# Optimization experiments

Measured on AMD Instinct MI355X. Metric: run time of the kernel, lower is better.

The kernel has to match this reference:

```python
import jax, jax.numpy as jnp
import numpy as np

EPS = 1e-5  # torch LayerNorm default eps
B, N, D_IN, E, H, V = 4096, 32, 256, 128, 512, 32

def _ln(x):
    # LayerNorm without affine (elementwise_affine=False), biased variance
    m = jnp.mean(x, axis=-1, keepdims=True)
    v = jnp.mean(jnp.square(x - m), axis=-1, keepdims=True)
    return (x - m) * jax.lax.rsqrt(v + EPS)

def _ln_gru_cell(x, h, i2h_W, i2h_b, h2h_W, h2h_b, hW_W, hW_b, hU_W, hU_b):
    gates = jax.nn.sigmoid(_ln(x @ i2h_W + i2h_b) + _ln(h @ h2h_W + h2h_b))  # [B,2H]
    hs = h.shape[-1]
    z_t = gates[:, :hs]
    r_t = gates[:, hs:]
    h_hat = jnp.tanh(_ln(x @ hW_W + hW_b) + r_t * _ln(h @ hU_W + hU_b))
    return (1.0 - z_t) * h + z_t * h_hat

def setup_inputs() -> dict:
    key = jax.random.key(0)
    ks = jax.random.split(key, 32)
    std0 = 1.0 / np.sqrt(H)
    u = lambda k, shp: jax.random.uniform(k, shp, jnp.float32, -std0, std0)
    in0 = 3 * E  # attn context + msg embedding + feedback embedding
    inp = {
        'sender_messages_embedded': jax.random.normal(ks[0], (B, E), jnp.float32),
        'prev_hidden': jax.random.normal(ks[1], (2, B, H), jnp.float32),
        'candidate_objects': jax.random.normal(ks[2], (B, N, D_IN), jnp.float32),
        'prev_msg_embedding': jax.random.normal(ks[3], (B, E), jnp.float32),
        # linear_objects_in_keys
        'Wk': jax.random.normal(ks[4], (D_IN, E), jnp.float32) * 0.05,
        'bk': jnp.zeros((E,), jnp.float32),
        # LayerNormGRUCell layer 0 (input 3E)
        'i2h_W0': u(ks[5], (in0, 2 * H)), 'i2h_b0': u(ks[6], (2 * H,)),
        'h2h_W0': u(ks[7], (H, 2 * H)), 'h2h_b0': u(ks[8], (2 * H,)),
        'hW_W0': u(ks[9], (in0, H)), 'hW_b0': u(ks[10], (H,)),
        'hU_W0': u(ks[11], (H, H)), 'hU_b0': u(ks[12], (H,)),
        # LayerNormGRUCell layer 1 (input H)
        'i2h_W1': u(ks[13], (H, 2 * H)), 'i2h_b1': u(ks[14], (2 * H,)),
        'h2h_W1': u(ks[15], (H, 2 * H)), 'h2h_b1': u(ks[16], (2 * H,)),
        'hW_W1': u(ks[17], (H, H)), 'hW_b1': u(ks[18], (H,)),
        'hU_W1': u(ks[19], (H, H)), 'hU_b1': u(ks[20], (H,)),
        # hidden_to_feedback_output
        'out_W': jax.random.normal(ks[21], (H, V), jnp.float32) * 0.05,
        'out_b': jnp.zeros((V,), jnp.float32),
    }
    return inp

def reference(sender_messages_embedded, prev_hidden, candidate_objects, prev_msg_embedding,
              Wk, bk,
              i2h_W0, i2h_b0, h2h_W0, h2h_b0, hW_W0, hW_b0, hU_W0, hU_b0,
              i2h_W1, i2h_b1, h2h_W1, h2h_b1, hW_W1, hW_b1, hU_W1, hU_b1,
              out_W, out_b):
    # object attention (dot): query = msg embedding, keys = projected candidates
    keys = candidate_objects @ Wk + bk                              # [B,N,E]
    scores = jnp.einsum('be,bne->bn', sender_messages_embedded, keys)
    weights = jax.nn.softmax(scores, axis=1)                        # [B,N]
    context = jnp.einsum('bn,bne->be', weights, keys)               # [B,E]
    rnn_input = jnp.concatenate([context, sender_messages_embedded, prev_msg_embedding], axis=-1)  # [B,3E]
    h0 = _ln_gru_cell(rnn_input, prev_hidden[0], i2h_W0, i2h_b0, h2h_W0, h2h_b0, hW_W0, hW_b0, hU_W0, hU_b0)
    h1 = _ln_gru_cell(h0, prev_hidden[1], i2h_W1, i2h_b1, h2h_W1, h2h_b1, hW_W1, hW_b1, hU_W1, hU_b1)
    logits = h1 @ out_W + out_b                                     # [B,V]
    logp = jax.nn.log_softmax(logits, axis=-1)
    probs = jnp.exp(logp)
    entropy = -jnp.sum(probs * logp, axis=-1)                       # [B]
    output_token = jnp.argmax(probs, axis=-1)                       # eval-mode argmax
    output_token_logits = jnp.take_along_axis(logp, output_token[:, None], axis=1)[:, 0]
    new_hidden = jnp.stack([h0, h1])                                # [2,B,H]
    return (output_token, entropy, output_token_logits, logits, new_hidden)
```

## Files before the change

kernel.cpp:

```cpp
#include <hip/hip_runtime.h>
#include <hip/hip_bf16.h>
#include <math.h>

#define B_SZ   4096
#define NCAND  32
#define DIN    256
#define E_SZ   128
#define H_SZ   512
#define VOCAB  32
#define LN_EPS 1e-5f

typedef unsigned short u16;
typedef unsigned int   u32;
typedef __attribute__((ext_vector_type(8))) short  short8;
typedef __attribute__((ext_vector_type(4))) float  floatx4;

static __device__ __forceinline__ float sigmoidf_(float x) {
    return 1.0f / (1.0f + expf(-x));
}
static __device__ __forceinline__ u16 f2bf(float x) {
    u32 u = __float_as_uint(x);
    return (u16)((u + 0x7FFFu + ((u >> 16) & 1u)) >> 16);
}
static __device__ __forceinline__ float bfbits2f(u16 h) {
    return __uint_as_float(((u32)h) << 16);
}

static __device__ __forceinline__ void split_store8(const float* __restrict__ g,
                                                    u16* __restrict__ sh,
                                                    u16* __restrict__ sl)
{
    float4 a = *(const float4*)g;
    float4 b = *(const float4*)(g + 4);
    float v[8] = {a.x, a.y, a.z, a.w, b.x, b.y, b.z, b.w};
    union { u16 us[8]; uint4 q; } hb, lb;
    #pragma unroll
    for (int j = 0; j < 8; ++j) {
        u16 h = f2bf(v[j]);
        hb.us[j] = h;
        lb.us[j] = f2bf(v[j] - bfbits2f(h));
    }
    *(uint4*)sh = hb.q;
    *(uint4*)sl = lb.q;
}

__global__ __launch_bounds__(256)
void transpose_split_w(const float* __restrict__ W1, const float* __restrict__ W2,
                       int N1, int N2, int K,
                       u16* __restrict__ Wt_hi, u16* __restrict__ Wt_lo)
{
    __shared__ float t[64][68];
    const int n0 = blockIdx.x * 64, k0 = blockIdx.y * 64;
    const int tid = threadIdx.x;

    {
        const int kl = tid >> 4, nl4 = (tid & 15) * 4;
        const int ng = n0 + nl4;
        const float* src; int col, ld;
        if (ng < N1) { src = W1; col = ng;      ld = N1; }
        else         { src = W2; col = ng - N1; ld = N2; }
        #pragma unroll
        for (int p = 0; p < 4; ++p) {
            float4 v = *(const float4*)(src + (size_t)(k0 + kl + p * 16) * ld + col);
            *(float4*)&t[kl + p * 16][nl4] = v;
        }
    }
    __syncthreads();

    const int nl = tid >> 2, kc = tid & 3;
    union { u16 us[16]; uint4 v[2]; } hb, lb;
    #pragma unroll
    for (int j = 0; j < 16; ++j) {
        float x = t[kc * 16 + j][nl];
        u16 h = f2bf(x);
        float r = x - bfbits2f(h);
        hb.us[j] = h;
        lb.us[j] = f2bf(r);
    }
    const size_t off = (size_t)(n0 + nl) * K + k0 + kc * 16;
    *(uint4*)(Wt_hi + off)     = hb.v[0];
    *(uint4*)(Wt_hi + off + 8) = hb.v[1];
    *(uint4*)(Wt_lo + off)     = lb.v[0];
    *(uint4*)(Wt_lo + off + 8) = lb.v[1];
}

__global__ __launch_bounds__(256)
void bias_cat_kernel(const float* __restrict__ b1, const float* __restrict__ b2,
                     int N1, int Ntot, float* __restrict__ out)
{
    int i = blockIdx.x * 256 + threadIdx.x;
    if (i < Ntot) out[i] = (i < N1) ? b1[i] : b2[i - N1];
}

__global__ __launch_bounds__(256)
void mfma_gemm_dual_kernel(const float* __restrict__ Ax, const u16* __restrict__ Wxh,
                           const u16* __restrict__ Wxl, const float* __restrict__ bx,
                           float* __restrict__ Cx, int Kx,
                           const float* __restrict__ Ahp, const u16* __restrict__ Whh,
                           const u16* __restrict__ Whl, const float* __restrict__ bh,
                           float* __restrict__ Ch, int Kh)
{
    __shared__ u16 sAh[128 * 40];
    __shared__ u16 sAl[128 * 40];
    __shared__ u16 sWh[128 * 40];
    __shared__ u16 sWl[128 * 40];

    const int tid  = threadIdx.x;
    const int lane = tid & 63;
    const int wave = tid >> 6;
    const int wm = (wave >> 1) * 64;
    const int wn = (wave & 1) * 64;
    const int r16 = lane & 15;
    const int q8  = (lane >> 4) * 8;

    const int sel    = blockIdx.y >> 5;
    const int m_base = (blockIdx.y & 31) * 128;
    const int n_base = blockIdx.x * 128;

    const float* A    = sel ? Ahp : Ax;
    const u16*   Wth  = sel ? Whh : Wxh;
    const u16*   Wtl  = sel ? Whl : Wxl;
    const float* bias = sel ? bh  : bx;
    float*       C    = sel ? Ch  : Cx;
    const int    K    = sel ? Kh  : Kx;

    const int row0 = tid >> 2,         col0 = (tid & 3) * 8;
    const int row1 = (tid + 256) >> 2, col1 = ((tid + 256) & 3) * 8;

    floatx4 acc[4][4] = {};

    for (int k0 = 0; k0 < K; k0 += 32) {
        {
            split_store8(A + (size_t)(m_base + row0) * K + k0 + col0,
                         &sAh[row0 * 40 + col0], &sAl[row0 * 40 + col0]);
            split_store8(A + (size_t)(m_base + row1) * K + k0 + col1,
                         &sAh[row1 * 40 + col1], &sAl[row1 * 40 + col1]);
            const size_t gW0 = (size_t)(n_base + row0) * K + k0 + col0;
            const size_t gW1 = (size_t)(n_base + row1) * K + k0 + col1;
            *(uint4*)&sWh[row0 * 40 + col0] = *(const uint4*)(Wth + gW0);
            *(uint4*)&sWh[row1 * 40 + col1] = *(const uint4*)(Wth + gW1);
            *(uint4*)&sWl[row0 * 40 + col0] = *(const uint4*)(Wtl + gW0);
            *(uint4*)&sWl[row1 * 40 + col1] = *(const uint4*)(Wtl + gW1);
        }
        __syncthreads();

        short8 ah[4], al[4], bhf[4], blf[4];
        #pragma unroll
        for (int i = 0; i < 4; ++i) {
            const int ar = (wm + i * 16 + r16) * 40 + q8;
            ah[i] = *(const short8*)&sAh[ar];
            al[i] = *(const short8*)&sAl[ar];
            const int br = (wn + i * 16 + r16) * 40 + q8;
            bhf[i] = *(const short8*)&sWh[br];
            blf[i] = *(const short8*)&sWl[br];
        }
        #pragma unroll
        for (int i = 0; i < 4; ++i)
            #pragma unroll
            for (int j = 0; j < 4; ++j) {
                acc[i][j] = __builtin_amdgcn_mfma_f32_16x16x32_bf16(ah[i], bhf[j], acc[i][j], 0, 0, 0);
                acc[i][j] = __builtin_amdgcn_mfma_f32_16x16x32_bf16(ah[i], blf[j], acc[i][j], 0, 0, 0);
                acc[i][j] = __builtin_amdgcn_mfma_f32_16x16x32_bf16(al[i], bhf[j], acc[i][j], 0, 0, 0);
            }
        __syncthreads();
    }

    const int quad = lane >> 4;
    #pragma unroll
    for (int j = 0; j < 4; ++j) {
        const int n = n_base + wn + j * 16 + r16;
        const float bv = bias[n];
        #pragma unroll
        for (int i = 0; i < 4; ++i) {
            #pragma unroll
            for (int r = 0; r < 4; ++r) {
                const int m = m_base + wm + i * 16 + quad * 4 + r;
                C[(size_t)m * 1536 + n] = acc[i][j][r] + bv;
            }
        }
    }
}

__global__ __launch_bounds__(256)
void gemm_bt64_kernel(const float* __restrict__ A, const float* __restrict__ Bt,
                      float* __restrict__ C, int M, int N, int K, int ldc)
{
    __shared__ float As[16][68];
    __shared__ float Bs[16][68];

    const int tid = threadIdx.x;
    const int bm = blockIdx.y * 64;
    const int bn = blockIdx.x * 64;
    const int tx = tid & 15, ty = tid >> 4;
    const int m0 = ty * 4, n0 = tx * 4;
    const int arow = tid >> 2, acol = (tid & 3) * 4;

    float acc[4][4] = {};

    for (int k0 = 0; k0 < K; k0 += 16) {
        float4 a4 = *(const float4*)(A  + (size_t)(bm + arow) * K + (k0 + acol));
        float4 b4 = *(const float4*)(Bt + (size_t)(bn + arow) * K + (k0 + acol));
        As[acol + 0][arow] = a4.x; As[acol + 1][arow] = a4.y;
        As[acol + 2][arow] = a4.z; As[acol + 3][arow] = a4.w;
        Bs[acol + 0][arow] = b4.x; Bs[acol + 1][arow] = b4.y;
        Bs[acol + 2][arow] = b4.z; Bs[acol + 3][arow] = b4.w;
        __syncthreads();
        #pragma unroll
        for (int k = 0; k < 16; ++k) {
            float4 av = *(const float4*)&As[k][m0];
            float4 bv = *(const float4*)&Bs[k][n0];
            float aa[4] = {av.x, av.y, av.z, av.w};
            float bb[4] = {bv.x, bv.y, bv.z, bv.w};
            #pragma unroll
            for (int i = 0; i < 4; ++i)
                #pragma unroll
                for (int j = 0; j < 4; ++j)
                    acc[i][j] = fmaf(aa[i], bb[j], acc[i][j]);
        }
        __syncthreads();
    }

    #pragma unroll
    for (int i = 0; i < 4; ++i)
        *(float4*)(C + (size_t)(bm + m0 + i) * ldc + bn + n0) =
            make_float4(acc[i][0], acc[i][1], acc[i][2], acc[i][3]);
}

__global__ __launch_bounds__(256)
void attn_ctx_kernel(const float* __restrict__ co, const float* __restrict__ q,
                     const float* __restrict__ snd, const float* __restrict__ pmsg,
                     float* __restrict__ cbar, float* __restrict__ rnn_in)
{
    __shared__ float s_co[NCAND][264];
    __shared__ float s_q[DIN];
    __shared__ float s_scores[NCAND];
    __shared__ float s_w[NCAND];

    const int b   = blockIdx.x;
    const int tid = threadIdx.x;

    {
        const float4* cop = (const float4*)(co + (size_t)b * NCAND * DIN);
        #pragma unroll
        for (int i = 0; i < 8; ++i) {
            int idx = tid + i * 256;
            float4 v = cop[idx];
            *(float4*)&s_co[idx >> 6][(idx & 63) * 4] = v;
        }
        if (tid < DIN) s_q[tid] = q[(size_t)b * DIN + tid];
    }
    __syncthreads();

    {
        const int n = tid >> 3, part = tid & 7;
        float sc = 0.f;
        #pragma unroll
        for (int qq = 0; qq < 8; ++qq) {
            const int d = part * 4 + qq * 32;
            float4 cv = *(const float4*)&s_co[n][d];
            float4 qv = *(const float4*)&s_q[d];
            sc += cv.x * qv.x + cv.y * qv.y + cv.z * qv.z + cv.w * qv.w;
        }
        #pragma unroll
        for (int m = 4; m; m >>= 1) sc += __shfl_xor(sc, m);
        if (part == 0) s_scores[n] = sc;
    }
    __syncthreads();

    if (tid < NCAND) {
        float s  = s_scores[tid];
        float mx = s;
        #pragma unroll
        for (int m = 16; m; m >>= 1) mx = fmaxf(mx, __shfl_xor(mx, m));
        float e = expf(s - mx);
        float sum = e;
        #pragma unroll
        for (int m = 16; m; m >>= 1) sum += __shfl_xor(sum, m);
        s_w[tid] = e / sum;
    }
    __syncthreads();

    {
        float cb = 0.f;
        #pragma unroll
        for (int n = 0; n < NCAND; ++n) cb = fmaf(s_w[n], s_co[n][tid], cb);
        cbar[(size_t)b * DIN + tid] = cb;
    }
    if (tid < 128)
        rnn_in[(size_t)b * 384 + 128 + tid] = snd[(size_t)b * E_SZ + tid];
    else
        rnn_in[(size_t)b * 384 + 128 + tid] = pmsg[(size_t)b * E_SZ + (tid - 128)];
}

__global__ __launch_bounds__(256)
void gemm_ctx_kernel(const float* __restrict__ A, const float* __restrict__ Bm,
                     const float* __restrict__ bias, float* __restrict__ C,
                     int M, int N, int K, int ldc)
{
    __shared__ float As[16][132];
    __shared__ float Bs[16][68];

    const int tid = threadIdx.x;
    const int bm = blockIdx.y * 128;
    const int bn = blockIdx.x * 64;
    const int tx = tid & 15, ty = tid >> 4;
    const int m0 = ty * 8, n0 = tx * 4;
    const int arow = tid >> 1, acol = (tid & 1) * 8;
    const int brow = tid >> 4, bcol = (tid & 15) * 4;

    float acc[8][4] = {};

    for (int k0 = 0; k0 < K; k0 += 16) {
        float4 a0 = *(const float4*)(A + (size_t)(bm + arow) * K + (k0 + acol));
        float4 a1 = *(const float4*)(A + (size_t)(bm + arow) * K + (k0 + acol + 4));
        float4 b4 = *(const float4*)(Bm + (size_t)(k0 + brow) * N + (bn + bcol));
        As[acol + 0][arow] = a0.x; As[acol + 1][arow] = a0.y;
        As[acol + 2][arow] = a0.z; As[acol + 3][arow] = a0.w;
        As[acol + 4][arow] = a1.x; As[acol + 5][arow] = a1.y;
        As[acol + 6][arow] = a1.z; As[acol + 7][arow] = a1.w;
        *(float4*)&Bs[brow][bcol] = b4;
        __syncthreads();
        #pragma unroll
        for (int k = 0; k < 16; ++k) {
            float4 av0 = *(const float4*)&As[k][m0];
            float4 av1 = *(const float4*)&As[k][m0 + 4];
            float4 bv  = *(const float4*)&Bs[k][n0];
            float aa[8] = {av0.x, av0.y, av0.z, av0.w, av1.x, av1.y, av1.z, av1.w};
            float bb[4] = {bv.x, bv.y, bv.z, bv.w};
            #pragma unroll
            for (int i = 0; i < 8; ++i)
                #pragma unroll
                for (int j = 0; j < 4; ++j)
                    acc[i][j] = fmaf(aa[i], bb[j], acc[i][j]);
        }
        __syncthreads();
    }

    const float4 bv = *(const float4*)(bias + bn + n0);
    #pragma unroll
    for (int i = 0; i < 8; ++i) {
        float4 o;
        o.x = acc[i][0] + bv.x; o.y = acc[i][1] + bv.y;
        o.z = acc[i][2] + bv.z; o.w = acc[i][3] + bv.w;
        *(float4*)(C + (size_t)(bm + m0 + i) * ldc + bn + n0) = o;
    }
}

__global__ __launch_bounds__(256)
void gru_combine_kernel(const float* __restrict__ gxc, const float* __restrict__ ghc,
                        const float* __restrict__ hprev, float* __restrict__ hout)
{
    const int b    = blockIdx.x;
    const int tid  = threadIdx.x;
    const int lane = tid & 63, wv = tid >> 6;

    __shared__ float s_part[4][8];
    __shared__ float s_gates[1024];

    const float* gxb = gxc + (size_t)b * 1536;
    const float* ghb = ghc + (size_t)b * 1536;

    const float4 gx4 = *(const float4*)(gxb + tid * 4);
    const float4 gh4 = *(const float4*)(ghb + tid * 4);
    const float2 cx2 = *(const float2*)(gxb + 1024 + tid * 2);
    const float2 ch2 = *(const float2*)(ghb + 1024 + tid * 2);

    float v[8];
    v[0] = gx4.x + gx4.y + gx4.z + gx4.w;
    v[1] = gx4.x*gx4.x + gx4.y*gx4.y + gx4.z*gx4.z + gx4.w*gx4.w;
    v[2] = gh4.x + gh4.y + gh4.z + gh4.w;
    v[3] = gh4.x*gh4.x + gh4.y*gh4.y + gh4.z*gh4.z + gh4.w*gh4.w;
    v[4] = cx2.x + cx2.y;
    v[5] = cx2.x*cx2.x + cx2.y*cx2.y;
    v[6] = ch2.x + ch2.y;
    v[7] = ch2.x*ch2.x + ch2.y*ch2.y;

    #pragma unroll
    for (int i = 0; i < 8; ++i)
        #pragma unroll
        for (int m = 32; m; m >>= 1) v[i] += __shfl_xor(v[i], m);

    if (lane == 0) {
        #pragma unroll
        for (int i = 0; i < 8; ++i) s_part[wv][i] = v[i];
    }
    __syncthreads();

    float t[8];
    #pragma unroll
    for (int i = 0; i < 8; ++i)
        t[i] = s_part[0][i] + s_part[1][i] + s_part[2][i] + s_part[3][i];

    const float mgx = t[0] / 1024.f;
    const float rgx = 1.f / sqrtf(t[1] / 1024.f - mgx * mgx + LN_EPS);
    const float mgh = t[2] / 1024.f;
    const float rgh = 1.f / sqrtf(t[3] / 1024.f - mgh * mgh + LN_EPS);
    const float mcx = t[4] / 512.f;
    const float rcx = 1.f / sqrtf(t[5] / 512.f - mcx * mcx + LN_EPS);
    const float mch = t[6] / 512.f;
    const float rch = 1.f / sqrtf(t[7] / 512.f - mch * mch + LN_EPS);

    float4 g;
    g.x = sigmoidf_((gx4.x - mgx) * rgx + (gh4.x - mgh) * rgh);
    g.y = sigmoidf_((gx4.y - mgx) * rgx + (gh4.y - mgh) * rgh);
    g.z = sigmoidf_((gx4.z - mgx) * rgx + (gh4.z - mgh) * rgh);
    g.w = sigmoidf_((gx4.w - mgx) * rgx + (gh4.w - mgh) * rgh);
    *(float4*)&s_gates[tid * 4] = g;
    __syncthreads();

    const float2 hp2 = *(const float2*)(hprev + (size_t)b * 512 + tid * 2);
    const float z0 = s_gates[tid * 2 + 0];
    const float z1 = s_gates[tid * 2 + 1];
    const float r0 = s_gates[512 + tid * 2 + 0];
    const float r1 = s_gates[512 + tid * 2 + 1];

    const float hh0 = tanhf((cx2.x - mcx) * rcx + r0 * ((ch2.x - mch) * rch));
    const float hh1 = tanhf((cx2.y - mcx) * rcx + r1 * ((ch2.y - mch) * rch));
    const float hn0 = (1.f - z0) * hp2.x + z0 * hh0;
    const float hn1 = (1.f - z1) * hp2.y + z1 * hh1;

    *(float2*)(hout + (size_t)b * 512 + tid * 2) = make_float2(hn0, hn1);
}

__global__ __launch_bounds__(256)
void out_kernel(const float* __restrict__ h1, const float* __restrict__ W,
                const float* __restrict__ bias, float* __restrict__ out)
{
    __shared__ float s_h[4][512];
    const int wave = threadIdx.x >> 6, lane = threadIdx.x & 63;
    const int b = blockIdx.x * 4 + wave;

    {
        const float4* hp = (const float4*)(h1 + (size_t)b * 512);
        float4* sp = (float4*)&s_h[wave][0];
        sp[lane]      = hp[lane];
        sp[lane + 64] = hp[lane + 64];
    }
    __syncthreads();

    const int v = lane & 31, half = lane >> 5;
    float acc = 0.f;
    {
        const float* wp = W + (size_t)half * 256 * 32 + v;
        const float* hh = &s_h[wave][half * 256];
        for (int k = 0; k < 256; ++k) acc = fmaf(hh[k], wp[(size_t)k * 32], acc);
    }
    acc += __shfl_xor(acc, 32);
    const float logit = acc + bias[v];

    if (half == 0)
        out[(size_t)3 * B_SZ + (size_t)b * VOCAB + v] = logit;

    float mval = logit; int midx = v;
    #pragma unroll
    for (int m = 16; m; m >>= 1) {
        float ov = __shfl_xor(mval, m);
        int   oi = __shfl_xor(midx, m);
        if (ov > mval || (ov == mval && oi < midx)) { mval = ov; midx = oi; }
    }
    float ex = expf(logit - mval);
    float sum = ex;
    #pragma unroll
    for (int m = 16; m; m >>= 1) sum += __shfl_xor(sum, m);
    const float lse  = mval + logf(sum);
    const float logp = logit - lse;
    const float p    = expf(logp);
    float epl = p * logp;
    #pragma unroll
    for (int m = 16; m; m >>= 1) epl += __shfl_xor(epl, m);
    const float entropy = -epl;
    const float tok_logp = __shfl(logp, midx, 32);

    if (lane == 0) {
        out[b]             = (float)midx;
        out[B_SZ + b]      = entropy;
        out[2 * B_SZ + b]  = tok_logp;
    }
}

extern "C" void kernel_launch(void* const* d_in, const int* in_sizes, int n_in,
                              void* d_out, int out_size, void* d_ws, size_t ws_size,
                              hipStream_t stream)
{
    const float* snd    = (const float*)d_in[0];
    const float* ph     = (const float*)d_in[1];
    const float* co     = (const float*)d_in[2];
    const float* pmsg   = (const float*)d_in[3];
    const float* Wk     = (const float*)d_in[4];
    const float* bk     = (const float*)d_in[5];
    const float* i2hW0  = (const float*)d_in[6];
    const float* i2hb0  = (const float*)d_in[7];
    const float* h2hW0  = (const float*)d_in[8];
    const float* h2hb0  = (const float*)d_in[9];
    const float* hWW0   = (const float*)d_in[10];
    const float* hWb0   = (const float*)d_in[11];
    const float* hUW0   = (const float*)d_in[12];
    const float* hUb0   = (const float*)d_in[13];
    const float* i2hW1  = (const float*)d_in[14];
    const float* i2hb1  = (const float*)d_in[15];
    const float* h2hW1  = (const float*)d_in[16];
    const float* h2hb1  = (const float*)d_in[17];
    const float* hWW1   = (const float*)d_in[18];
    const float* hWb1   = (const float*)d_in[19];
    const float* hUW1   = (const float*)d_in[20];
    const float* hUb1   = (const float*)d_in[21];
    const float* outW   = (const float*)d_in[22];
    const float* outb   = (const float*)d_in[23];

    float* out = (float*)d_out;
    float* h0out = out + (size_t)3 * B_SZ + (size_t)B_SZ * VOCAB;
    float* h1out = h0out + (size_t)B_SZ * H_SZ;

    const float* h0prev = ph;
    const float* h1prev = ph + (size_t)B_SZ * H_SZ;

    char* p = (char*)d_ws;
    auto alloc_f = [&](size_t n) { float* r = (float*)p; p += n * 4; return r; };
    auto alloc_h = [&](size_t n) { u16* r = (u16*)p; p += ((n * 2 + 15) & ~15ull); return r; };

    float* qbuf   = alloc_f((size_t)B_SZ * 256);
    float* cbar   = alloc_f((size_t)B_SZ * 256);
    float* rnn_in = alloc_f((size_t)B_SZ * 384);
    float* gxc    = alloc_f((size_t)B_SZ * 1536);
    float* ghc    = alloc_f((size_t)B_SZ * 1536);
    u16* W0x_hi = alloc_h((size_t)1536 * 384);
    u16* W0x_lo = alloc_h((size_t)1536 * 384);
    u16* W0h_hi = alloc_h((size_t)1536 * 512);
    u16* W0h_lo = alloc_h((size_t)1536 * 512);
    u16* W1x_hi = alloc_h((size_t)1536 * 512);
    u16* W1x_lo = alloc_h((size_t)1536 * 512);
    u16* W1h_hi = alloc_h((size_t)1536 * 512);
    u16* W1h_lo = alloc_h((size_t)1536 * 512);
    float* b0x = alloc_f(1536);
    float* b0h = alloc_f(1536);
    float* b1x = alloc_f(1536);
    float* b1h = alloc_f(1536);

    transpose_split_w<<<dim3(24, 6), 256, 0, stream>>>(i2hW0, hWW0, 1024, 512, 384, W0x_hi, W0x_lo);
    transpose_split_w<<<dim3(24, 8), 256, 0, stream>>>(h2hW0, hUW0, 1024, 512, 512, W0h_hi, W0h_lo);
    transpose_split_w<<<dim3(24, 8), 256, 0, stream>>>(i2hW1, hWW1, 1024, 512, 512, W1x_hi, W1x_lo);
    transpose_split_w<<<dim3(24, 8), 256, 0, stream>>>(h2hW1, hUW1, 1024, 512, 512, W1h_hi, W1h_lo);
    bias_cat_kernel<<<6, 256, 0, stream>>>(i2hb0, hWb0, 1024, 1536, b0x);
    bias_cat_kernel<<<6, 256, 0, stream>>>(h2hb0, hUb0, 1024, 1536, b0h);
    bias_cat_kernel<<<6, 256, 0, stream>>>(i2hb1, hWb1, 1024, 1536, b1x);
    bias_cat_kernel<<<6, 256, 0, stream>>>(h2hb1, hUb1, 1024, 1536, b1h);

    gemm_bt64_kernel<<<dim3(4, 64), 256, 0, stream>>>(snd, Wk, qbuf, B_SZ, 256, 128, 256);
    attn_ctx_kernel<<<B_SZ, 256, 0, stream>>>(co, qbuf, snd, pmsg, cbar, rnn_in);
    gemm_ctx_kernel<<<dim3(2, 32), 256, 0, stream>>>(cbar, Wk, bk, rnn_in, B_SZ, 128, 256, 384);

    mfma_gemm_dual_kernel<<<dim3(12, 64), 256, 0, stream>>>(
        rnn_in, W0x_hi, W0x_lo, b0x, gxc, 384,
        ph,     W0h_hi, W0h_lo, b0h, ghc, 512);
    gru_combine_kernel<<<B_SZ, 256, 0, stream>>>(gxc, ghc, h0prev, h0out);

    mfma_gemm_dual_kernel<<<dim3(12, 64), 256, 0, stream>>>(
        h0out,                    W1x_hi, W1x_lo, b1x, gxc, 512,
        ph + (size_t)B_SZ * 512,  W1h_hi, W1h_lo, b1h, ghc, 512);
    gru_combine_kernel<<<B_SZ, 256, 0, stream>>>(gxc, ghc, h1prev, h1out);

    out_kernel<<<B_SZ / 4, 256, 0, stream>>>(h1out, outW, outb, out);
}
```

Before: 468.8 us.

## Pre-split GEMM operands into tile-blocked bf16 images loaded via global_load_lds

Activations (rnn input, previous hidden states, h0) are now split into bf16 hi/lo pairs by their producing kernels and stored in a 128x32 tile-blocked layout, so the dual MFMA GEMM no longer converts fp32 to bf16 in its main loop. The GEMM stages tiles with direct global-to-LDS loads and drops the padded LDS stride. The four bias concatenations are also merged into one launch. In exchange the producers do extra writes, an extra split kernel runs over prev_hidden, and the unpadded LDS rows may cause bank conflicts when fragments are read.

After: 452.3 us. 3.5% less time.

```diff
diff --git a/kernel.cpp b/kernel.cpp
--- a/kernel.cpp
+++ b/kernel.cpp
@@ -26,6 +26,12 @@
     return __uint_as_float(((u32)h) << 16);
 }
 
+typedef const __attribute__((address_space(1))) unsigned int* gas_ptr;
+typedef __attribute__((address_space(3)))       unsigned int* las_ptr;
+static __device__ __forceinline__ void gload_lds16(const u16* g, u16* l) {
+    __builtin_amdgcn_global_load_lds((gas_ptr)(const void*)g, (las_ptr)(void*)l, 16, 0, 0);
+}
+
 static __device__ __forceinline__ void split_store8(const float* __restrict__ g,
                                                     u16* __restrict__ sh,
                                                     u16* __restrict__ sl)
@@ -44,6 +50,7 @@
     *(uint4*)sl = lb.q;
 }
 
+
 __global__ __launch_bounds__(256)
 void transpose_split_w(const float* __restrict__ W1, const float* __restrict__ W2,
                        int N1, int N2, int K,
@@ -52,6 +59,7 @@
     __shared__ float t[64][68];
     const int n0 = blockIdx.x * 64, k0 = blockIdx.y * 64;
     const int tid = threadIdx.x;
+    const int KT = K >> 5;
 
     {
         const int kl = tid >> 4, nl4 = (tid & 15) * 4;
@@ -77,7 +85,10 @@
         hb.us[j] = h;
         lb.us[j] = f2bf(r);
     }
-    const size_t off = (size_t)(n0 + nl) * K + k0 + kc * 16;
+    const int n  = n0 + nl;
+    const int kb = k0 + kc * 16;
+    const size_t off = ((size_t)(n >> 7) * KT + (kb >> 5)) * 4096
+                     + (size_t)(n & 127) * 32 + (kb & 31);
     *(uint4*)(Wt_hi + off)     = hb.v[0];
     *(uint4*)(Wt_hi + off + 8) = hb.v[1];
     *(uint4*)(Wt_lo + off)     = lb.v[0];
@@ -85,25 +96,45 @@
 }
 
 __global__ __launch_bounds__(256)
-void bias_cat_kernel(const float* __restrict__ b1, const float* __restrict__ b2,
-                     int N1, int Ntot, float* __restrict__ out)
-{
-    int i = blockIdx.x * 256 + threadIdx.x;
-    if (i < Ntot) out[i] = (i < N1) ? b1[i] : b2[i - N1];
-}
-
-__global__ __launch_bounds__(256)
-void mfma_gemm_dual_kernel(const float* __restrict__ Ax, const u16* __restrict__ Wxh,
-                           const u16* __restrict__ Wxl, const float* __restrict__ bx,
-                           float* __restrict__ Cx, int Kx,
-                           const float* __restrict__ Ahp, const u16* __restrict__ Whh,
-                           const u16* __restrict__ Whl, const float* __restrict__ bh,
-                           float* __restrict__ Ch, int Kh)
-{
-    __shared__ u16 sAh[128 * 40];
-    __shared__ u16 sAl[128 * 40];
-    __shared__ u16 sWh[128 * 40];
-    __shared__ u16 sWl[128 * 40];
+void bias_cat4_kernel(const float* __restrict__ a0, const float* __restrict__ c0, float* __restrict__ o0,
+                      const float* __restrict__ a1, const float* __restrict__ c1, float* __restrict__ o1,
+                      const float* __restrict__ a2, const float* __restrict__ c2, float* __restrict__ o2,
+                      const float* __restrict__ a3, const float* __restrict__ c3, float* __restrict__ o3)
+{
+    const int t = blockIdx.x * 256 + threadIdx.x;
+    const int w = t / 1536;
+    const int i = t - w * 1536;
+    const float* a; const float* c; float* o;
+    if      (w == 0) { a = a0; c = c0; o = o0; }
+    else if (w == 1) { a = a1; c = c1; o = o1; }
+    else if (w == 2) { a = a2; c = c2; o = o2; }
+    else             { a = a3; c = c3; o = o3; }
+    o[i] = (i < 1024) ? a[i] : c[i - 1024];
+}
+
+__global__ __launch_bounds__(256)
+void split_blocked_kernel(const float* __restrict__ src,
+                          u16* __restrict__ hi, u16* __restrict__ lo)
+{
+    const int i = blockIdx.x * 256 + threadIdx.x;
+    const int m = i >> 6, kq = (i & 63) << 3;
+    const size_t idx = ((size_t)(m >> 7) * 16 + (kq >> 5)) * 4096
+                     + (size_t)(m & 127) * 32 + (kq & 31);
+    split_store8(src + (size_t)m * 512 + kq, &hi[idx], &lo[idx]);
+}
+
+__global__ __launch_bounds__(256)
+void mfma_gemm_dual_kernel(const u16* __restrict__ Axh, const u16* __restrict__ Axl,
+                           const u16* __restrict__ Wxh, const u16* __restrict__ Wxl,
+                           const float* __restrict__ bx, float* __restrict__ Cx, int KTx,
+                           const u16* __restrict__ Ahh, const u16* __restrict__ Ahl,
+                           const u16* __restrict__ Whh, const u16* __restrict__ Whl,
+                           const float* __restrict__ bh, float* __restrict__ Ch, int KTh)
+{
+    __shared__ __align__(16) u16 sAh[128 * 32];
+    __shared__ __align__(16) u16 sAl[128 * 32];
+    __shared__ __align__(16) u16 sWh[128 * 32];
+    __shared__ __align__(16) u16 sWl[128 * 32];
 
     const int tid  = threadIdx.x;
     const int lane = tid & 63;
@@ -117,40 +148,43 @@
     const int m_base = (blockIdx.y & 31) * 128;
     const int n_base = blockIdx.x * 128;
 
-    const float* A    = sel ? Ahp : Ax;
-    const u16*   Wth  = sel ? Whh : Wxh;
-    const u16*   Wtl  = sel ? Whl : Wxl;
-    const float* bias = sel ? bh  : bx;
-    float*       C    = sel ? Ch  : Cx;
-    const int    K    = sel ? Kh  : Kx;
-
-    const int row0 = tid >> 2,         col0 = (tid & 3) * 8;
-    const int row1 = (tid + 256) >> 2, col1 = ((tid + 256) & 3) * 8;
+    const u16* Ah_  = sel ? Ahh : Axh;
+    const u16* Al_  = sel ? Ahl : Axl;
+    const u16* Wh_  = sel ? Whh : Wxh;
+    const u16* Wl_  = sel ? Whl : Wxl;
+    const float* bias = sel ? bh : bx;
+    float*       C    = sel ? Ch : Cx;
+    const int    KT   = sel ? KTh : KTx;
+
+    const size_t abase = (size_t)(m_base >> 7) * KT * 4096;
+    const size_t wbase = (size_t)(n_base >> 7) * KT * 4096;
+    const int sofs = wave * 1024;
+    const int gofs = sofs + (lane << 3);
 
     floatx4 acc[4][4] = {};
 
-    for (int k0 = 0; k0 < K; k0 += 32) {
+    for (int kt = 0; kt < KT; ++kt) {
         {
-            split_store8(A + (size_t)(m_base + row0) * K + k0 + col0,
-                         &sAh[row0 * 40 + col0], &sAl[row0 * 40 + col0]);
-            split_store8(A + (size_t)(m_base + row1) * K + k0 + col1,
-                         &sAh[row1 * 40 + col1], &sAl[row1 * 40 + col1]);
-            const size_t gW0 = (size_t)(n_base + row0) * K + k0 + col0;
-            const size_t gW1 = (size_t)(n_base + row1) * K + k0 + col1;
-            *(uint4*)&sWh[row0 * 40 + col0] = *(const uint4*)(Wth + gW0);
-            *(uint4*)&sWh[row1 * 40 + col1] = *(const uint4*)(Wth + gW1);
-            *(uint4*)&sWl[row0 * 40 + col0] = *(const uint4*)(Wtl + gW0);
-            *(uint4*)&sWl[row1 * 40 + col1] = *(const uint4*)(Wtl + gW1);
+            const size_t ai = abase + (size_t)kt * 4096 + gofs;
+            const size_t wi = wbase + (size_t)kt * 4096 + gofs;
+            gload_lds16(Ah_ + ai,       &sAh[sofs]);
+            gload_lds16(Ah_ + ai + 512, &sAh[sofs + 512]);
+            gload_lds16(Al_ + ai,       &sAl[sofs]);
+            gload_lds16(Al_ + ai + 512, &sAl[sofs + 512]);
+            gload_lds16(Wh_ + wi,       &sWh[sofs]);
+            gload_lds16(Wh_ + wi + 512, &sWh[sofs + 512]);
+            gload_lds16(Wl_ + wi,       &sWl[sofs]);
+            gload_lds16(Wl_ + wi + 512, &sWl[sofs + 512]);
         }
         __syncthreads();
 
         short8 ah[4], al[4], bhf[4], blf[4];
         #pragma unroll
         for (int i = 0; i < 4; ++i) {
-            const int ar = (wm + i * 16 + r16) * 40 + q8;
+            const int ar = (wm + i * 16 + r16) * 32 + q8;
             ah[i] = *(const short8*)&sAh[ar];
             al[i] = *(const short8*)&sAl[ar];
-            const int br = (wn + i * 16 + r16) * 40 + q8;
+            const int br = (wn + i * 16 + r16) * 32 + q8;
             bhf[i] = *(const short8*)&sWh[br];
             blf[i] = *(const short8*)&sWl[br];
         }
@@ -229,7 +263,8 @@
 __global__ __launch_bounds__(256)
 void attn_ctx_kernel(const float* __restrict__ co, const float* __restrict__ q,
                      const float* __restrict__ snd, const float* __restrict__ pmsg,
-                     float* __restrict__ cbar, float* __restrict__ rnn_in)
+                     float* __restrict__ cbar,
+                     u16* __restrict__ rinh, u16* __restrict__ rinl)
 {
     __shared__ float s_co[NCAND][264];
     __shared__ float s_q[DIN];
@@ -286,16 +321,24 @@
         for (int n = 0; n < NCAND; ++n) cb = fmaf(s_w[n], s_co[n][tid], cb);
         cbar[(size_t)b * DIN + tid] = cb;
     }
-    if (tid < 128)
-        rnn_in[(size_t)b * 384 + 128 + tid] = snd[(size_t)b * E_SZ + tid];
-    else
-        rnn_in[(size_t)b * 384 + 128 + tid] = pmsg[(size_t)b * E_SZ + (tid - 128)];
+    {
+        const float x = (tid < 128) ? snd[(size_t)b * E_SZ + tid]
+                                    : pmsg[(size_t)b * E_SZ + (tid - 128)];
+        const int d = 128 + tid;
+        const u16 h = f2bf(x);
+        const u16 l = f2bf(x - bfbits2f(h));
+        const size_t idx = ((size_t)(b >> 7) * 12 + (d >> 5)) * 4096
+                         + (size_t)(b & 127) * 32 + (d & 31);
+        rinh[idx] = h;
+        rinl[idx] = l;
+    }
 }
 
 __global__ __launch_bounds__(256)
 void gemm_ctx_kernel(const float* __restrict__ A, const float* __restrict__ Bm,
-                     const float* __restrict__ bias, float* __restrict__ C,
-                     int M, int N, int K, int ldc)
+                     const float* __restrict__ bias,
+                     u16* __restrict__ rinh, u16* __restrict__ rinl,
+                     int M, int N, int K)
 {
     __shared__ float As[16][132];
     __shared__ float Bs[16][68];
@@ -339,16 +382,29 @@
     const float4 bv = *(const float4*)(bias + bn + n0);
     #pragma unroll
     for (int i = 0; i < 8; ++i) {
-        float4 o;
-        o.x = acc[i][0] + bv.x; o.y = acc[i][1] + bv.y;
-        o.z = acc[i][2] + bv.z; o.w = acc[i][3] + bv.w;
-        *(float4*)(C + (size_t)(bm + m0 + i) * ldc + bn + n0) = o;
+        float o0 = acc[i][0] + bv.x, o1 = acc[i][1] + bv.y;
+        float o2 = acc[i][2] + bv.z, o3 = acc[i][3] + bv.w;
+        const int m = bm + m0 + i;
+        const int d = bn + n0;
+        const u16 h0 = f2bf(o0), h1 = f2bf(o1), h2 = f2bf(o2), h3 = f2bf(o3);
+        const u16 l0 = f2bf(o0 - bfbits2f(h0));
+        const u16 l1 = f2bf(o1 - bfbits2f(h1));
+        const u16 l2 = f2bf(o2 - bfbits2f(h2));
+        const u16 l3 = f2bf(o3 - bfbits2f(h3));
+        const size_t idx = ((size_t)(m >> 7) * 12 + (d >> 5)) * 4096
+                         + (size_t)(m & 127) * 32 + (d & 31);
+        uint2 hv, lv;
+        hv.x = (u32)h0 | ((u32)h1 << 16); hv.y = (u32)h2 | ((u32)h3 << 16);
+        lv.x = (u32)l0 | ((u32)l1 << 16); lv.y = (u32)l2 | ((u32)l3 << 16);
+        *(uint2*)&rinh[idx] = hv;
+        *(uint2*)&rinl[idx] = lv;
     }
 }
 
 __global__ __launch_bounds__(256)
 void gru_combine_kernel(const float* __restrict__ gxc, const float* __restrict__ ghc,
-                        const float* __restrict__ hprev, float* __restrict__ hout)
+                        const float* __restrict__ hprev, float* __restrict__ hout,
+                        u16* __restrict__ himg_hi, u16* __restrict__ himg_lo)
 {
     const int b    = blockIdx.x;
     const int tid  = threadIdx.x;
@@ -420,6 +476,17 @@
     const float hn1 = (1.f - z1) * hp2.y + z1 * hh1;
 
     *(float2*)(hout + (size_t)b * 512 + tid * 2) = make_float2(hn0, hn1);
+
+    if (himg_hi) {
+        const u16 h0b = f2bf(hn0), h1b = f2bf(hn1);
+        const u16 l0b = f2bf(hn0 - bfbits2f(h0b));
+        const u16 l1b = f2bf(hn1 - bfbits2f(h1b));
+        const int k = tid * 2;
+        const size_t idx = ((size_t)(b >> 7) * 16 + (k >> 5)) * 4096
+                         + (size_t)(b & 127) * 32 + (k & 31);
+        *(u32*)&himg_hi[idx] = (u32)h0b | ((u32)h1b << 16);
+        *(u32*)&himg_lo[idx] = (u32)l0b | ((u32)l1b << 16);
+    }
 }
 
 __global__ __launch_bounds__(256)
@@ -520,9 +587,14 @@
 
     float* qbuf   = alloc_f((size_t)B_SZ * 256);
     float* cbar   = alloc_f((size_t)B_SZ * 256);
-    float* rnn_in = alloc_f((size_t)B_SZ * 384);
     float* gxc    = alloc_f((size_t)B_SZ * 1536);
     float* ghc    = alloc_f((size_t)B_SZ * 1536);
+    u16* rin_hi = alloc_h((size_t)B_SZ * 384);
+    u16* rin_lo = alloc_h((size_t)B_SZ * 384);
+    u16* php_hi = alloc_h((size_t)2 * B_SZ * 512);
+    u16* php_lo = alloc_h((size_t)2 * B_SZ * 512);
+    u16* h0i_hi = alloc_h((size_t)B_SZ * 512);
+    u16* h0i_lo = alloc_h((size_t)B_SZ * 512);
     u16* W0x_hi = alloc_h((size_t)1536 * 384);
     u16* W0x_lo = alloc_h((size_t)1536 * 384);
     u16* W0h_hi = alloc_h((size_t)1536 * 512);
@@ -540,24 +612,24 @@
     transpose_split_w<<<dim3(24, 8), 256, 0, stream>>>(h2hW0, hUW0, 1024, 512, 512, W0h_hi, W0h_lo);
     transpose_split_w<<<dim3(24, 8), 256, 0, stream>>>(i2hW1, hWW1, 1024, 512, 512, W1x_hi, W1x_lo);
     transpose_split_w<<<dim3(24, 8), 256, 0, stream>>>(h2hW1, hUW1, 1024, 512, 512, W1h_hi, W1h_lo);
-    bias_cat_kernel<<<6, 256, 0, stream>>>(i2hb0, hWb0, 1024, 1536, b0x);
-    bias_cat_kernel<<<6, 256, 0, stream>>>(h2hb0, hUb0, 1024, 1536, b0h);
-    bias_cat_kernel<<<6, 256, 0, stream>>>(i2hb1, hWb1, 1024, 1536, b1x);
-    bias_cat_kernel<<<6, 256, 0, stream>>>(h2hb1, hUb1, 1024, 1536, b1h);
+    bias_cat4_kernel<<<24, 256, 0, stream>>>(i2hb0, hWb0, b0x, h2hb0, hUb0, b0h,
+                                             i2hb1, hWb1, b1x, h2hb1, hUb1, b1h);
+    split_blocked_kernel<<<2 * B_SZ * 64 / 256, 256, 0, stream>>>(ph, php_hi, php_lo);
 
     gemm_bt64_kernel<<<dim3(4, 64), 256, 0, stream>>>(snd, Wk, qbuf, B_SZ, 256, 128, 256);
-    attn_ctx_kernel<<<B_SZ, 256, 0, stream>>>(co, qbuf, snd, pmsg, cbar, rnn_in);
-    gemm_ctx_kernel<<<dim3(2, 32), 256, 0, stream>>>(cbar, Wk, bk, rnn_in, B_SZ, 128, 256, 384);
+    attn_ctx_kernel<<<B_SZ, 256, 0, stream>>>(co, qbuf, snd, pmsg, cbar, rin_hi, rin_lo);
+    gemm_ctx_kernel<<<dim3(2, 32), 256, 0, stream>>>(cbar, Wk, bk, rin_hi, rin_lo, B_SZ, 128, 256);
 
     mfma_gemm_dual_kernel<<<dim3(12, 64), 256, 0, stream>>>(
-        rnn_in, W0x_hi, W0x_lo, b0x, gxc, 384,
-        ph,     W0h_hi, W0h_lo, b0h, ghc, 512);
-    gru_combine_kernel<<<B_SZ, 256, 0, stream>>>(gxc, ghc, h0prev, h0out);
+        rin_hi, rin_lo, W0x_hi, W0x_lo, b0x, gxc, 12,
+        php_hi, php_lo, W0h_hi, W0h_lo, b0h, ghc, 16);
+    gru_combine_kernel<<<B_SZ, 256, 0, stream>>>(gxc, ghc, h0prev, h0out, h0i_hi, h0i_lo);
 
     mfma_gemm_dual_kernel<<<dim3(12, 64), 256, 0, stream>>>(
-        h0out,                    W1x_hi, W1x_lo, b1x, gxc, 512,
-        ph + (size_t)B_SZ * 512,  W1h_hi, W1h_lo, b1h, ghc, 512);
-    gru_combine_kernel<<<B_SZ, 256, 0, stream>>>(gxc, ghc, h1prev, h1out);
+        h0i_hi, h0i_lo, W1x_hi, W1x_lo, b1x, gxc, 16,
+        php_hi + (size_t)B_SZ * 512, php_lo + (size_t)B_SZ * 512,
+        W1h_hi, W1h_lo, b1h, ghc, 16);
+    gru_combine_kernel<<<B_SZ, 256, 0, stream>>>(gxc, ghc, h1prev, h1out, (u16*)nullptr, (u16*)nullptr);
 
     out_kernel<<<B_SZ / 4, 256, 0, stream>>>(h1out, outW, outb, out);
 }
```
